# Performance work log

Measured on AMD Instinct MI355X. Metric: run time of the kernel, lower is better.

## Reference

```python
import jax, jax.numpy as jnp
import numpy as np

INPUT_DIM = 2304
SUBSPACE_DIM = 64
ATOMS = 512
NUM_EXPERTS = 256
K = 4


def leaky_offset_relu(x, negative_slope, offset):
    return jnp.where(x >= offset, x, negative_slope * x)


def setup_inputs() -> dict:
    key = jax.random.key(0)
    k0, k1, k2, k3 = jax.random.split(key, 4)
    x = jax.random.normal(k0, (INPUT_DIM,), dtype=jnp.float32)
    # top-level autoencoder encoder (he_uniform approximated by scaled normal)
    enc_top = jax.random.normal(k1, (NUM_EXPERTS, INPUT_DIM), dtype=jnp.float32) * (1.0 / np.sqrt(INPUT_DIM))
    # per-expert down-projection, row-normalized as in __init__
    W_down = jax.random.normal(k2, (NUM_EXPERTS, SUBSPACE_DIM, INPUT_DIM), dtype=jnp.float32)
    W_down = W_down / jnp.linalg.norm(W_down, axis=-1, keepdims=True)
    # per-expert encoder weights, row-normalized as in __init__
    encoder_weights = jax.random.normal(k3, (NUM_EXPERTS, ATOMS, SUBSPACE_DIM), dtype=jnp.float32)
    encoder_weights = encoder_weights / jnp.linalg.norm(encoder_weights, axis=-1, keepdims=True)
    return {"x": x, "enc_top": enc_top, "W_down": W_down, "encoder_weights": encoder_weights}


def reference(x, enc_top, W_down, encoder_weights):
    offset_top = 1.0 / jnp.sqrt(jnp.float32(INPUT_DIM))
    # --- top-level encode: codes = relu_offset(E @ x), negative_slope=0.0 ---
    codes = leaky_offset_relu(enc_top @ x, 0.0, offset_top)  # [num_experts]
    # --- top-k routing (naive_top_k == top_k on a single row) ---
    top_k_values, top_k_indices = jax.lax.top_k(codes, K)  # [k], [k]
    # --- gather per-expert weights, dispatch, expert compute ---
    sel_W_down = W_down[top_k_indices]            # [k, sub, in]
    sel_enc = encoder_weights[top_k_indices]      # [k, atoms, sub]
    subspace_outputs = jnp.einsum('ksd,d->ks', sel_W_down, x)        # [k, sub]
    expert_codes = jnp.einsum('kas,ks->ka', sel_enc, subspace_outputs)  # [k, atoms]
    expert_codes = leaky_offset_relu(expert_codes, 0.01, offset_top)
    # --- decode: top-level decoder is encoder^T; select columns by indices ---
    top_level_output = jnp.einsum('kd,k->d', enc_top[top_k_indices], top_k_values)  # [in]
    # expert decoders are encoder^T, W_up is W_down^T (weight tying)
    decoded_subspace = jnp.einsum('kas,ka->ks', sel_enc, expert_codes)  # [k, sub]
    reconstructed = jnp.einsum('ksd,ks->d', sel_W_down, decoded_subspace)  # sum over experts -> [in]
    return reconstructed + top_level_output
```

## Files before the change

### kernel.cpp

```cpp
#include <hip/hip_runtime.h>
#include <float.h>

#define INPUT_DIM 2304
#define SUB_DIM 64
#define ATOMS 512
#define NUM_EXPERTS 256
#define TOPK 4

#define OFFSET (1.0f / 48.0f)
#define MAGIC 0x9E3779B9u

typedef unsigned long long u64;

__device__ __forceinline__ u64 pair_ld(const u64* p) {
    return __hip_atomic_load(p, __ATOMIC_RELAXED, __HIP_MEMORY_SCOPE_AGENT);
}
__device__ __forceinline__ void pair_st(u64* p, u64 v) {
    __hip_atomic_store(p, v, __ATOMIC_RELAXED, __HIP_MEMORY_SCOPE_AGENT);
}
__device__ __forceinline__ u64 pack(float f) {
    return ((u64)__float_as_uint(f) << 32) | (u64)MAGIC;
}
__device__ __forceinline__ bool pvalid(u64 v) { return (unsigned)v == MAGIC; }
__device__ __forceinline__ float payload(u64 v) { return __uint_as_float((unsigned)(v >> 32)); }
__device__ __forceinline__ float dot4(float4 a, float4 b) {
    return a.x * b.x + a.y * b.y + a.z * b.z + a.w * b.w;
}


__global__ void __launch_bounds__(256, 1) moe_fused(
    const float* __restrict__ x,
    const float* __restrict__ enc_top,
    const float* __restrict__ W_down,
    const float* __restrict__ enc_w,
    float* __restrict__ out,
    float* __restrict__ ws_f)
{
    u64* pc = (u64*)ws_f;
    u64* ps = pc + 256 * 256;
    u64* pd = ps + 2 * 256;

    __shared__ float s_red[256];
    __shared__ float s_bc;
    __shared__ float s_sub[SUB_DIM];
    __shared__ float s_ec[256];
    __shared__ float s_decp[16][SUB_DIM];
    __shared__ float s_dec[SUB_DIM];
    __shared__ int   s_idx[TOPK];
    __shared__ float s_val[TOPK];

    const int b    = blockIdx.x;
    const int t    = threadIdx.x;
    const int lane = t & 63;
    const int wave = t >> 6;
    const float4* x4 = (const float4*)x;

    {
        const float4* row4 = (const float4*)(enc_top + (size_t)b * INPUT_DIM);
        float acc = dot4(row4[t], x4[t]) + dot4(row4[t + 256], x4[t + 256]);
        if (t < 64) acc += dot4(row4[t + 512], x4[t + 512]);
        #pragma unroll
        for (int o = 32; o > 0; o >>= 1) acc += __shfl_down(acc, o);
        if (lane == 0) s_red[wave] = acc;
        __syncthreads();
        if (t == 0) {
            float s = s_red[0] + s_red[1] + s_red[2] + s_red[3];
            s_bc = (s >= OFFSET) ? s : 0.0f;
        }
        __syncthreads();
        pair_st(&pc[(size_t)t * 256 + b], pack(s_bc));
    }

    if (wave == 0) {
        u64 v0, v1, v2, v3;
        for (;;) {
            v0 = pair_ld(&pc[(size_t)b * 256 + lane]);
            v1 = pair_ld(&pc[(size_t)b * 256 + lane + 64]);
            v2 = pair_ld(&pc[(size_t)b * 256 + lane + 128]);
            v3 = pair_ld(&pc[(size_t)b * 256 + lane + 192]);
            if (__all(pvalid(v0) && pvalid(v1) && pvalid(v2) && pvalid(v3))) break;
        }
        float v[4] = { payload(v0), payload(v1), payload(v2), payload(v3) };
        int   id[4] = { lane, lane + 64, lane + 128, lane + 192 };
        for (int k = 0; k < TOPK; ++k) {
            float bv = v[0]; int bi = id[0];
            #pragma unroll
            for (int i = 1; i < 4; ++i)
                if (v[i] > bv || (v[i] == bv && id[i] < bi)) { bv = v[i]; bi = id[i]; }
            #pragma unroll
            for (int o = 32; o > 0; o >>= 1) {
                float ov = __shfl_down(bv, o);
                int   oi = __shfl_down(bi, o);
                if (ov > bv || (ov == bv && oi < bi)) { bv = ov; bi = oi; }
            }
            bv = __shfl(bv, 0);
            bi = __shfl(bi, 0);
            if (lane == 0) { s_idx[k] = bi; s_val[k] = bv; }
            #pragma unroll
            for (int i = 0; i < 4; ++i)
                if (id[i] == bi) v[i] = -FLT_MAX;
        }
        pair_st(&pc[(size_t)b * 256 + lane], 0ull);
        pair_st(&pc[(size_t)b * 256 + lane + 64], 0ull);
        pair_st(&pc[(size_t)b * 256 + lane + 128], 0ull);
        pair_st(&pc[(size_t)b * 256 + lane + 192], 0ull);
    }
    __syncthreads();

    const float* Wexp = nullptr;
    float pf = 0.0f;
    if (b < 8) {
        const int e = b >> 1, h = b & 1;
        Wexp = enc_w + (size_t)s_idx[e] * ATOMS * SUB_DIM + (size_t)h * 256 * SUB_DIM;
        #pragma unroll
        for (int i = 0; i < 4; ++i) {
            float4 w = ((const float4*)Wexp)[(size_t)(t + i * 256) * 4];
            pf += w.x + w.y + w.z + w.w;
        }
    }

    {
        const int E = s_idx[b >> 6];
        const float4* row4 = (const float4*)(W_down + ((size_t)E * SUB_DIM + (b & 63)) * INPUT_DIM);
        float acc = dot4(row4[t], x4[t]) + dot4(row4[t + 256], x4[t + 256]);
        if (t < 64) acc += dot4(row4[t + 512], x4[t + 512]);
        #pragma unroll
        for (int o = 32; o > 0; o >>= 1) acc += __shfl_down(acc, o);
        if (lane == 0) s_red[wave] = acc;
        __syncthreads();
        if (t == 0) {
            float s = s_red[0] + s_red[1] + s_red[2] + s_red[3];
            const u64 pv = pack(s);
            pair_st(&ps[b], pv);
            pair_st(&ps[256 + b], pv);
        }
    }

    if (b >= 44) return;

    if (b < 8) {
        const int e = b >> 1, h = b & 1;
        if (wave == 0) {
            u64 v;
            for (;;) {
                v = pair_ld(&ps[h * 256 + e * SUB_DIM + lane]);
                if (__all(pvalid(v))) break;
            }
            s_sub[lane] = payload(v);
            pair_st(&ps[h * 256 + e * SUB_DIM + lane], 0ull);
        }
        asm volatile("" :: "v"(pf));
        __syncthreads();
        {
            const float4* row4 = (const float4*)(Wexp + (size_t)t * SUB_DIM);
            float acc = 0.0f;
            #pragma unroll
            for (int i = 0; i < SUB_DIM / 4; ++i) {
                float4 w = row4[i];
                acc += w.x * s_sub[4*i] + w.y * s_sub[4*i+1] + w.z * s_sub[4*i+2] + w.w * s_sub[4*i+3];
            }
            s_ec[t] = (acc >= OFFSET) ? acc : 0.01f * acc;
        }
        __syncthreads();
        {
            const int sg = t & 15, ch = t >> 4;
            float4 a4 = make_float4(0.f, 0.f, 0.f, 0.f);
            for (int aa = ch * 16; aa < ch * 16 + 16; ++aa) {
                float4 w = *(const float4*)(Wexp + (size_t)aa * SUB_DIM + sg * 4);
                float  ec = s_ec[aa];
                a4.x += w.x * ec; a4.y += w.y * ec; a4.z += w.z * ec; a4.w += w.w * ec;
            }
            *(float4*)&s_decp[ch][sg * 4] = a4;
        }
        __syncthreads();
        if (t < SUB_DIM) {
            float d = 0.0f;
            #pragma unroll
            for (int c = 0; c < 16; ++c) d += s_decp[c][t];
            s_dec[t] = d;
        }
        __syncthreads();
        {
            const u64 pv = pack(s_dec[lane]);
            #pragma unroll
            for (int i = 0; i < 9; ++i) {
                const int r = wave + 4 * i;
                pair_st(&pd[(((size_t)r * TOPK + e) * 2 + h) * 64 + lane], pv);
            }
        }
        return;
    }

    {
        const int rb = b - 8;
        const int d  = rb * 64 + lane;
        const int E  = s_idx[wave];
        float wr[SUB_DIM];
        const float* Wb = W_down + (size_t)E * SUB_DIM * INPUT_DIM + d;
        #pragma unroll
        for (int s = 0; s < SUB_DIM; ++s) wr[s] = Wb[(size_t)s * INPUT_DIM];
        const float et = s_val[wave] * enc_top[(size_t)E * INPUT_DIM + d];
        u64 v0, v1;
        for (;;) {
            v0 = pair_ld(&pd[(((size_t)rb * TOPK + wave) * 2 + 0) * 64 + lane]);
            v1 = pair_ld(&pd[(((size_t)rb * TOPK + wave) * 2 + 1) * 64 + lane]);
            if (__all(pvalid(v0) && pvalid(v1))) break;
        }
        float dv = payload(v0) + payload(v1);
        pair_st(&pd[(((size_t)rb * TOPK + wave) * 2 + 0) * 64 + lane], 0ull);
        pair_st(&pd[(((size_t)rb * TOPK + wave) * 2 + 1) * 64 + lane], 0ull);
        float acc = et;
        #pragma unroll
        for (int s = 0; s < SUB_DIM; ++s)
            acc += wr[s] * __shfl(dv, s);
        s_red[t] = acc;
        __syncthreads();
        if (t < 64)
            out[rb * 64 + t] = s_red[t] + s_red[t + 64] + s_red[t + 128] + s_red[t + 192];
    }
}

extern "C" void kernel_launch(void* const* d_in, const int* in_sizes, int n_in,
                              void* d_out, int out_size, void* d_ws, size_t ws_size,
                              hipStream_t stream) {
    const float* x       = (const float*)d_in[0];
    const float* enc_top = (const float*)d_in[1];
    const float* W_down  = (const float*)d_in[2];
    const float* enc_w   = (const float*)d_in[3];
    float* out = (float*)d_out;
    float* ws  = (float*)d_ws;

    moe_fused<<<dim3(256), dim3(256), 0, stream>>>(x, enc_top, W_down, enc_w, out, ws);
}
```

Baseline: 17.33 us.

## Add dedicated expert blocks splitting encoder work into quarters across 16 extra blocks

Result: slower. 17.84 us (+3.0%).

```diff
diff --git a/kernel.cpp b/kernel.cpp
--- a/kernel.cpp
+++ b/kernel.cpp
@@ -6,6 +6,8 @@
 #define ATOMS 512
 #define NUM_EXPERTS 256
 #define TOPK 4
+#define NBLK 272
+#define NREADER 288
 
 #define OFFSET (1.0f / 48.0f)
 #define MAGIC 0x9E3779B9u
@@ -37,13 +39,12 @@
     float* __restrict__ ws_f)
 {
     u64* pc = (u64*)ws_f;
-    u64* ps = pc + 256 * 256;
-    u64* pd = ps + 2 * 256;
+    u64* ps = pc + (size_t)NREADER * 256;
+    u64* pd = ps + 4 * 256;
 
     __shared__ float s_red[256];
-    __shared__ float s_bc;
     __shared__ float s_sub[SUB_DIM];
-    __shared__ float s_ec[256];
+    __shared__ float s_ec[128];
     __shared__ float s_decp[16][SUB_DIM];
     __shared__ float s_dec[SUB_DIM];
     __shared__ int   s_idx[TOPK];
@@ -55,104 +56,178 @@
     const int wave = t >> 6;
     const float4* x4 = (const float4*)x;
 
+    if (b < 256) {
+        {
+            const float4* row4 = (const float4*)(enc_top + (size_t)b * INPUT_DIM);
+            float acc = dot4(row4[t], x4[t]) + dot4(row4[t + 256], x4[t + 256]);
+            if (t < 64) acc += dot4(row4[t + 512], x4[t + 512]);
+            #pragma unroll
+            for (int o = 32; o > 0; o >>= 1) acc += __shfl_down(acc, o);
+            if (lane == 0) s_red[wave] = acc;
+            __syncthreads();
+            float c = (s_red[0] + s_red[1]) + (s_red[2] + s_red[3]);
+            c = (c >= OFFSET) ? c : 0.0f;
+            const u64 pv = pack(c);
+            pair_st(&pc[(size_t)t * 256 + b], pv);
+            if (t < 16) pair_st(&pc[(size_t)(256 + t) * 256 + b], pv);
+        }
+
+        if (wave == 0) {
+            u64 v0, v1, v2, v3;
+            for (;;) {
+                v0 = pair_ld(&pc[(size_t)b * 256 + lane]);
+                v1 = pair_ld(&pc[(size_t)b * 256 + lane + 64]);
+                v2 = pair_ld(&pc[(size_t)b * 256 + lane + 128]);
+                v3 = pair_ld(&pc[(size_t)b * 256 + lane + 192]);
+                if (__all(pvalid(v0) && pvalid(v1) && pvalid(v2) && pvalid(v3))) break;
+            }
+            float v[4] = { payload(v0), payload(v1), payload(v2), payload(v3) };
+            int   id[4] = { lane, lane + 64, lane + 128, lane + 192 };
+            for (int k = 0; k < TOPK; ++k) {
+                float bv = v[0]; int bi = id[0];
+                #pragma unroll
+                for (int i = 1; i < 4; ++i)
+                    if (v[i] > bv || (v[i] == bv && id[i] < bi)) { bv = v[i]; bi = id[i]; }
+                #pragma unroll
+                for (int o = 32; o > 0; o >>= 1) {
+                    float ov = __shfl_down(bv, o);
+                    int   oi = __shfl_down(bi, o);
+                    if (ov > bv || (ov == bv && oi < bi)) { bv = ov; bi = oi; }
+                }
+                bv = __shfl(bv, 0);
+                bi = __shfl(bi, 0);
+                if (lane == 0) { s_idx[k] = bi; s_val[k] = bv; }
+                #pragma unroll
+                for (int i = 0; i < 4; ++i)
+                    if (id[i] == bi) v[i] = -FLT_MAX;
+            }
+            pair_st(&pc[(size_t)b * 256 + lane], 0ull);
+            pair_st(&pc[(size_t)b * 256 + lane + 64], 0ull);
+            pair_st(&pc[(size_t)b * 256 + lane + 128], 0ull);
+            pair_st(&pc[(size_t)b * 256 + lane + 192], 0ull);
+        }
+        __syncthreads();
+
+        {
+            const int E = s_idx[b >> 6];
+            const float4* row4 = (const float4*)(W_down + ((size_t)E * SUB_DIM + (b & 63)) * INPUT_DIM);
+            float acc = dot4(row4[t], x4[t]) + dot4(row4[t + 256], x4[t + 256]);
+            if (t < 64) acc += dot4(row4[t + 512], x4[t + 512]);
+            #pragma unroll
+            for (int o = 32; o > 0; o >>= 1) acc += __shfl_down(acc, o);
+            if (lane == 0) s_red[wave] = acc;
+            __syncthreads();
+            float s = (s_red[0] + s_red[1]) + (s_red[2] + s_red[3]);
+            if (t < 4) pair_st(&ps[(size_t)t * 256 + b], pack(s));
+        }
+
+        if (b >= 36) return;
+
+        {
+            __syncthreads();
+            const int rb = b;
+            const int d  = rb * 64 + lane;
+            const int E  = s_idx[wave];
+            float wr[SUB_DIM];
+            const float* Wb = W_down + (size_t)E * SUB_DIM * INPUT_DIM + d;
+            #pragma unroll
+            for (int s = 0; s < SUB_DIM; ++s) wr[s] = Wb[(size_t)s * INPUT_DIM];
+            const float et = s_val[wave] * enc_top[(size_t)E * INPUT_DIM + d];
+            const size_t base = ((size_t)rb * TOPK + wave) * 4 * 64 + lane;
+            u64 v0, v1, v2, v3;
+            for (;;) {
+                v0 = pair_ld(&pd[base]);
+                v1 = pair_ld(&pd[base + 64]);
+                v2 = pair_ld(&pd[base + 128]);
+                v3 = pair_ld(&pd[base + 192]);
+                if (__all(pvalid(v0) && pvalid(v1) && pvalid(v2) && pvalid(v3))) break;
+            }
+            float dv = (payload(v0) + payload(v1)) + (payload(v2) + payload(v3));
+            pair_st(&pd[base], 0ull);
+            pair_st(&pd[base + 64], 0ull);
+            pair_st(&pd[base + 128], 0ull);
+            pair_st(&pd[base + 192], 0ull);
+            float a0 = 0.f, a1 = 0.f, a2 = 0.f, a3 = 0.f;
+            #pragma unroll
+            for (int s = 0; s < SUB_DIM; s += 4) {
+                a0 += wr[s]     * __shfl(dv, s);
+                a1 += wr[s + 1] * __shfl(dv, s + 1);
+                a2 += wr[s + 2] * __shfl(dv, s + 2);
+                a3 += wr[s + 3] * __shfl(dv, s + 3);
+            }
+            s_red[t] = et + ((a0 + a1) + (a2 + a3));
+            __syncthreads();
+            if (t < 64)
+                out[rb * 64 + t] = s_red[t] + s_red[t + 64] + s_red[t + 128] + s_red[t + 192];
+        }
+        return;
+    }
+
     {
-        const float4* row4 = (const float4*)(enc_top + (size_t)b * INPUT_DIM);
-        float acc = dot4(row4[t], x4[t]) + dot4(row4[t + 256], x4[t + 256]);
-        if (t < 64) acc += dot4(row4[t + 512], x4[t + 512]);
-        #pragma unroll
-        for (int o = 32; o > 0; o >>= 1) acc += __shfl_down(acc, o);
-        if (lane == 0) s_red[wave] = acc;
-        __syncthreads();
-        if (t == 0) {
-            float s = s_red[0] + s_red[1] + s_red[2] + s_red[3];
-            s_bc = (s >= OFFSET) ? s : 0.0f;
-        }
-        __syncthreads();
-        pair_st(&pc[(size_t)t * 256 + b], pack(s_bc));
-    }
-
-    if (wave == 0) {
-        u64 v0, v1, v2, v3;
-        for (;;) {
-            v0 = pair_ld(&pc[(size_t)b * 256 + lane]);
-            v1 = pair_ld(&pc[(size_t)b * 256 + lane + 64]);
-            v2 = pair_ld(&pc[(size_t)b * 256 + lane + 128]);
-            v3 = pair_ld(&pc[(size_t)b * 256 + lane + 192]);
-            if (__all(pvalid(v0) && pvalid(v1) && pvalid(v2) && pvalid(v3))) break;
-        }
-        float v[4] = { payload(v0), payload(v1), payload(v2), payload(v3) };
-        int   id[4] = { lane, lane + 64, lane + 128, lane + 192 };
-        for (int k = 0; k < TOPK; ++k) {
-            float bv = v[0]; int bi = id[0];
-            #pragma unroll
-            for (int i = 1; i < 4; ++i)
-                if (v[i] > bv || (v[i] == bv && id[i] < bi)) { bv = v[i]; bi = id[i]; }
-            #pragma unroll
-            for (int o = 32; o > 0; o >>= 1) {
-                float ov = __shfl_down(bv, o);
-                int   oi = __shfl_down(bi, o);
-                if (ov > bv || (ov == bv && oi < bi)) { bv = ov; bi = oi; }
-            }
-            bv = __shfl(bv, 0);
-            bi = __shfl(bi, 0);
-            if (lane == 0) { s_idx[k] = bi; s_val[k] = bv; }
-            #pragma unroll
-            for (int i = 0; i < 4; ++i)
-                if (id[i] == bi) v[i] = -FLT_MAX;
-        }
-        pair_st(&pc[(size_t)b * 256 + lane], 0ull);
-        pair_st(&pc[(size_t)b * 256 + lane + 64], 0ull);
-        pair_st(&pc[(size_t)b * 256 + lane + 128], 0ull);
-        pair_st(&pc[(size_t)b * 256 + lane + 192], 0ull);
-    }
-    __syncthreads();
-
-    const float* Wexp = nullptr;
-    float pf = 0.0f;
-    if (b < 8) {
-        const int e = b >> 1, h = b & 1;
-        Wexp = enc_w + (size_t)s_idx[e] * ATOMS * SUB_DIM + (size_t)h * 256 * SUB_DIM;
-        #pragma unroll
-        for (int i = 0; i < 4; ++i) {
-            float4 w = ((const float4*)Wexp)[(size_t)(t + i * 256) * 4];
-            pf += w.x + w.y + w.z + w.w;
-        }
-    }
-
-    {
-        const int E = s_idx[b >> 6];
-        const float4* row4 = (const float4*)(W_down + ((size_t)E * SUB_DIM + (b & 63)) * INPUT_DIM);
-        float acc = dot4(row4[t], x4[t]) + dot4(row4[t + 256], x4[t + 256]);
-        if (t < 64) acc += dot4(row4[t + 512], x4[t + 512]);
-        #pragma unroll
-        for (int o = 32; o > 0; o >>= 1) acc += __shfl_down(acc, o);
-        if (lane == 0) s_red[wave] = acc;
-        __syncthreads();
-        if (t == 0) {
-            float s = s_red[0] + s_red[1] + s_red[2] + s_red[3];
-            const u64 pv = pack(s);
-            pair_st(&ps[b], pv);
-            pair_st(&ps[256 + b], pv);
-        }
-    }
-
-    if (b >= 44) return;
-
-    if (b < 8) {
-        const int e = b >> 1, h = b & 1;
+        const int eb = b - 256;
+        const int e  = eb >> 2;
+        const int q  = eb & 3;
+
+        if (wave == 0) {
+            u64 v0, v1, v2, v3;
+            for (;;) {
+                v0 = pair_ld(&pc[(size_t)b * 256 + lane]);
+                v1 = pair_ld(&pc[(size_t)b * 256 + lane + 64]);
+                v2 = pair_ld(&pc[(size_t)b * 256 + lane + 128]);
+                v3 = pair_ld(&pc[(size_t)b * 256 + lane + 192]);
+                if (__all(pvalid(v0) && pvalid(v1) && pvalid(v2) && pvalid(v3))) break;
+            }
+            float v[4] = { payload(v0), payload(v1), payload(v2), payload(v3) };
+            int   id[4] = { lane, lane + 64, lane + 128, lane + 192 };
+            for (int k = 0; k < TOPK; ++k) {
+                float bv = v[0]; int bi = id[0];
+                #pragma unroll
+                for (int i = 1; i < 4; ++i)
+                    if (v[i] > bv || (v[i] == bv && id[i] < bi)) { bv = v[i]; bi = id[i]; }
+                #pragma unroll
+                for (int o = 32; o > 0; o >>= 1) {
+                    float ov = __shfl_down(bv, o);
+                    int   oi = __shfl_down(bi, o);
+                    if (ov > bv || (ov == bv && oi < bi)) { bv = ov; bi = oi; }
+                }
+                bv = __shfl(bv, 0);
+                bi = __shfl(bi, 0);
+                if (lane == 0) { s_idx[k] = bi; s_val[k] = bv; }
+                #pragma unroll
+                for (int i = 0; i < 4; ++i)
+                    if (id[i] == bi) v[i] = -FLT_MAX;
+            }
+            pair_st(&pc[(size_t)b * 256 + lane], 0ull);
+            pair_st(&pc[(size_t)b * 256 + lane + 64], 0ull);
+            pair_st(&pc[(size_t)b * 256 + lane + 128], 0ull);
+            pair_st(&pc[(size_t)b * 256 + lane + 192], 0ull);
+        }
+        __syncthreads();
+
+        const int E = s_idx[e];
+        const float* Wq = enc_w + ((size_t)E * ATOMS + (size_t)q * 128) * SUB_DIM;
+
+        float pf = 0.0f;
+        {
+            float4 w0 = ((const float4*)Wq)[(size_t)(t * 2) * 4];
+            float4 w1 = ((const float4*)Wq)[(size_t)(t * 2 + 1) * 4];
+            pf = w0.x + w0.w + w1.x + w1.w;
+        }
+
         if (wave == 0) {
             u64 v;
             for (;;) {
-                v = pair_ld(&ps[h * 256 + e * SUB_DIM + lane]);
+                v = pair_ld(&ps[(size_t)q * 256 + e * SUB_DIM + lane]);
                 if (__all(pvalid(v))) break;
             }
             s_sub[lane] = payload(v);
-            pair_st(&ps[h * 256 + e * SUB_DIM + lane], 0ull);
+            pair_st(&ps[(size_t)q * 256 + e * SUB_DIM + lane], 0ull);
         }
         asm volatile("" :: "v"(pf));
         __syncthreads();
-        {
-            const float4* row4 = (const float4*)(Wexp + (size_t)t * SUB_DIM);
+
+        if (t < 128) {
+            const float4* row4 = (const float4*)(Wq + (size_t)t * SUB_DIM);
             float acc = 0.0f;
             #pragma unroll
             for (int i = 0; i < SUB_DIM / 4; ++i) {
@@ -162,11 +237,13 @@
             s_ec[t] = (acc >= OFFSET) ? acc : 0.01f * acc;
         }
         __syncthreads();
+
         {
             const int sg = t & 15, ch = t >> 4;
             float4 a4 = make_float4(0.f, 0.f, 0.f, 0.f);
-            for (int aa = ch * 16; aa < ch * 16 + 16; ++aa) {
-                float4 w = *(const float4*)(Wexp + (size_t)aa * SUB_DIM + sg * 4);
+            #pragma unroll
+            for (int aa = ch * 8; aa < ch * 8 + 8; ++aa) {
+                float4 w = *(const float4*)(Wq + (size_t)aa * SUB_DIM + sg * 4);
                 float  ec = s_ec[aa];
                 a4.x += w.x * ec; a4.y += w.y * ec; a4.z += w.z * ec; a4.w += w.w * ec;
             }
@@ -174,49 +251,21 @@
         }
         __syncthreads();
         if (t < SUB_DIM) {
-            float d = 0.0f;
-            #pragma unroll
-            for (int c = 0; c < 16; ++c) d += s_decp[c][t];
-            s_dec[t] = d;
-        }
-        __syncthreads();
+            float dsum = 0.0f;
+            #pragma unroll
+            for (int c = 0; c < 16; ++c) dsum += s_decp[c][t];
+            s_dec[t] = dsum;
+        }
+        __syncthreads();
+
         {
             const u64 pv = pack(s_dec[lane]);
             #pragma unroll
             for (int i = 0; i < 9; ++i) {
                 const int r = wave + 4 * i;
-                pair_st(&pd[(((size_t)r * TOPK + e) * 2 + h) * 64 + lane], pv);
-            }
-        }
-        return;
-    }
-
-    {
-        const int rb = b - 8;
-        const int d  = rb * 64 + lane;
-        const int E  = s_idx[wave];
-        float wr[SUB_DIM];
-        const float* Wb = W_down + (size_t)E * SUB_DIM * INPUT_DIM + d;
-        #pragma unroll
-        for (int s = 0; s < SUB_DIM; ++s) wr[s] = Wb[(size_t)s * INPUT_DIM];
-        const float et = s_val[wave] * enc_top[(size_t)E * INPUT_DIM + d];
-        u64 v0, v1;
-        for (;;) {
-            v0 = pair_ld(&pd[(((size_t)rb * TOPK + wave) * 2 + 0) * 64 + lane]);
-            v1 = pair_ld(&pd[(((size_t)rb * TOPK + wave) * 2 + 1) * 64 + lane]);
-            if (__all(pvalid(v0) && pvalid(v1))) break;
-        }
-        float dv = payload(v0) + payload(v1);
-        pair_st(&pd[(((size_t)rb * TOPK + wave) * 2 + 0) * 64 + lane], 0ull);
-        pair_st(&pd[(((size_t)rb * TOPK + wave) * 2 + 1) * 64 + lane], 0ull);
-        float acc = et;
-        #pragma unroll
-        for (int s = 0; s < SUB_DIM; ++s)
-            acc += wr[s] * __shfl(dv, s);
-        s_red[t] = acc;
-        __syncthreads();
-        if (t < 64)
-            out[rb * 64 + t] = s_red[t] + s_red[t + 64] + s_red[t + 128] + s_red[t + 192];
+                pair_st(&pd[(((size_t)r * TOPK + e) * 4 + q) * 64 + lane], pv);
+            }
+        }
     }
 }
 
@@ -230,5 +279,5 @@
     float* out = (float*)d_out;
     float* ws  = (float*)d_ws;
 
-    moe_fused<<<dim3(256), dim3(256), 0, stream>>>(x, enc_top, W_down, enc_w, out, ws);
-}
+    moe_fused<<<dim3(NBLK), dim3(256), 0, stream>>>(x, enc_top, W_down, enc_w, out, ws);
+}
```
